# Performance work log

Measured on AMD Instinct MI355X. Metric: run time of the kernel, lower is better.

Reference implementation:

```python
import jax, jax.numpy as jnp
import numpy as np

SMU_ALPHA = 0.25
SMU_MU = 1.0e6  # repo's act.SMU default: large mu -> smooth leaky-relu (max(x, alpha*x))

def smu(x):
    a = SMU_ALPHA
    return 0.5 * ((1.0 + a) * x + (1.0 - a) * x * jax.lax.erf(SMU_MU * (1.0 - a) * x))

def setup_inputs() -> dict:
    key = jax.random.key(0)
    ks = jax.random.split(key, 6)
    B, N, D = 8, 4096, 1024
    xavier = float(np.sqrt(6.0 / (D + D)))
    def lin_w(k):
        return jax.random.uniform(k, (D, D), jnp.float32, -xavier, xavier)
    return {
        "x": jax.random.normal(ks[0], (B, N, D), jnp.float32),
        "Wvr": lin_w(ks[1]), "bvr": jnp.zeros((D,), jnp.float32),
        "Wvi": lin_w(ks[2]), "bvi": jnp.zeros((D,), jnp.float32),
        "Wk": lin_w(ks[3]), "bk": jnp.zeros((D,), jnp.float32),
        "Wq": lin_w(ks[4]), "bq": jnp.zeros((D,), jnp.float32),
    }

def reference(x, Wvr, bvr, Wvi, bvi, Wk, bk, Wq, bq):
    # real input: real and imag branches both see x
    value_real = jnp.einsum('bnd,ed->bne', x, Wvr) + bvr
    value_imag = jnp.einsum('bnd,ed->bne', x, Wvi) + bvi
    # GLU: v_real * tanh(softplus(v_imag)); dropout disabled (p=0)
    value = value_real * jnp.tanh(jax.nn.softplus(value_imag))
    key_ = jnp.einsum('bnd,ed->bne', x, Wk) + bk
    query = jnp.einsum('bnd,ed->bne', x, Wq) + bq
    # L2 normalize along the sequence dim (dim=1)
    key_n = key_ / (jnp.linalg.norm(key_, axis=1, keepdims=True) + 1e-5)
    query_n = query / (jnp.linalg.norm(query, axis=1, keepdims=True) + 1e-5)
    feature_attn = smu(jnp.einsum('bnd,bne->bde', key_n, query_n))  # [B, D, D]
    return jnp.einsum('bnd,bde->bne', value, feature_attn)
```

## Files before the change

kernel.cpp:

```cpp
#include <hip/hip_runtime.h>
#include <math.h>

typedef __bf16 bf16x8 __attribute__((ext_vector_type(8)));
typedef float f32x4 __attribute__((ext_vector_type(4)));

#define MTOT 32768
#define DD   1024
#define NSEQ 4096
#define BB   8

__device__ __forceinline__ void async16(const void* gp, void* lp) {
  __builtin_amdgcn_global_load_lds(
      (__attribute__((address_space(1))) void*)(const_cast<void*>(gp)),
      (__attribute__((address_space(3))) void*)(lp), 16, 0, 0);
}

__device__ __forceinline__ unsigned short f2bf(float f) {
  union { float f; unsigned int u; } v; v.f = f;
  unsigned int r = v.u + 0x7fffu + ((v.u >> 16) & 1u);
  return (unsigned short)(r >> 16);
}
__device__ __forceinline__ float bf2f(unsigned short u) {
  union { unsigned int u; float f; } v; v.u = ((unsigned int)u) << 16; return v.f;
}

__global__ void cvt_bf16(const float* __restrict__ in, unsigned short* __restrict__ out, int n) {
  int i = (blockIdx.x * blockDim.x + threadIdx.x) * 8;
  if (i >= n) return;
  float4 a = *(const float4*)(in + i);
  float4 b = *(const float4*)(in + i + 4);
  ushort4 o0, o1;
  o0.x = f2bf(a.x); o0.y = f2bf(a.y); o0.z = f2bf(a.z); o0.w = f2bf(a.w);
  o1.x = f2bf(b.x); o1.y = f2bf(b.y); o1.z = f2bf(b.z); o1.w = f2bf(b.w);
  *(ushort4*)(out + i) = o0;
  *(ushort4*)(out + i + 4) = o1;
}

__global__ void cvt_w(const float* __restrict__ w0, const float* __restrict__ w1,
                      const float* __restrict__ w2, const float* __restrict__ w3,
                      unsigned short* __restrict__ out) {
  int z = blockIdx.y;
  const float* in = (z == 0) ? w0 : (z == 1) ? w1 : (z == 2) ? w2 : w3;
  int i = (blockIdx.x * blockDim.x + threadIdx.x) * 8;
  float4 a = *(const float4*)(in + i);
  float4 b = *(const float4*)(in + i + 4);
  ushort4 o0, o1;
  o0.x = f2bf(a.x); o0.y = f2bf(a.y); o0.z = f2bf(a.z); o0.w = f2bf(a.w);
  o1.x = f2bf(b.x); o1.y = f2bf(b.y); o1.z = f2bf(b.z); o1.w = f2bf(b.w);
  unsigned short* o = out + (size_t)z * DD * DD;
  *(ushort4*)(o + i) = o0;
  *(ushort4*)(o + i + 4) = o1;
}

__device__ __forceinline__ void stage_half(const unsigned short* __restrict__ g,
                                           int row0, int k0,
                                           unsigned short* lds, int tid) {
#pragma unroll
  for (int l = 0; l < 2; ++l) {
    int u = l * 512 + tid;
    int r = u >> 3;
    int sl = (u & 7) ^ (r & 7);
    async16(g + (size_t)(row0 + r) * 1024 + k0 + sl * 8, (char*)lds + u * 16);
  }
}

__global__ __launch_bounds__(512, 2) void proj_all(
    const unsigned short* __restrict__ xb,
    const unsigned short* __restrict__ Wb,
    const float* __restrict__ bvr, const float* __restrict__ bvi,
    const float* __restrict__ bk,  const float* __restrict__ bq,
    unsigned short* __restrict__ oVr, unsigned short* __restrict__ oVi,
    unsigned short* __restrict__ Kt,  unsigned short* __restrict__ Qt,
    float* __restrict__ rnacc) {
  __shared__ __align__(16) unsigned short smem[65536];

  const int bx = blockIdx.x;
  const int swz = (bx & 7) * 64 + (bx >> 3);
  const int m0 = (swz >> 2) * 256;
  const int n0 = (swz & 3) * 256;
  const int z = blockIdx.z;
  const unsigned short* W = Wb + (size_t)z * DD * DD;
  const float* bias = (z == 0) ? bvr : (z == 1) ? bvi : (z == 2) ? bk : bq;

  const int tid = threadIdx.x;
  const int w = tid >> 6, lane = tid & 63;
  const int wr = w >> 2, wc = w & 3;
  const int lq = lane >> 4, lr = lane & 15;
  const int sx = lr & 7;
  const int arow0 = wr * 128 + lr;
  const int brow0 = wc * 64 + lr;

  f32x4 acc[8][4];
#pragma unroll
  for (int i = 0; i < 8; i++)
#pragma unroll
    for (int j = 0; j < 4; j++) acc[i][j] = (f32x4)(0.f);

  const int NT = 16;

  stage_half(xb, m0,       0,  smem,                     tid);
  stage_half(xb, m0 + 128, 0,  smem + 8192,              tid);
  stage_half(W,  n0,       0,  smem + 16384,             tid);
  stage_half(W,  n0 + 128, 0,  smem + 16384 + 8192,      tid);
  stage_half(W,  n0,       64, smem + 32768 + 16384,     tid);
  stage_half(W,  n0 + 128, 64, smem + 32768 + 16384 + 8192, tid);
  asm volatile("s_waitcnt vmcnt(4)" ::: "memory");
  __builtin_amdgcn_s_barrier();

  for (int t = 0; t < NT; ++t) {
    const unsigned short* As = smem + (t & 1) * 32768;
    const unsigned short* Bs = As + 16384;
    bf16x8 bfr[4][2];
#pragma unroll
    for (int q = 0; q < 4; ++q) {
      bf16x8 afq[2][2];
      if (q == 0) {
#pragma unroll
        for (int nj = 0; nj < 4; ++nj)
#pragma unroll
          for (int ks = 0; ks < 2; ++ks)
            bfr[nj][ks] = *(const bf16x8*)(Bs + (brow0 + nj * 16) * 64 +
                                           ((((ks << 2) | lq) ^ sx) << 3));
      }
#pragma unroll
      for (int mi = 0; mi < 2; ++mi)
#pragma unroll
        for (int ks = 0; ks < 2; ++ks)
          afq[mi][ks] = *(const bf16x8*)(As + (arow0 + (2 * q + mi) * 16) * 64 +
                                         ((((ks << 2) | lq) ^ sx) << 3));
      if (q == 0) {
        if (t + 1 < NT)
          stage_half(xb, m0, (t + 1) * 64, smem + ((t + 1) & 1) * 32768, tid);
      } else if (q == 1) {
        if (t + 1 < NT)
          stage_half(xb, m0 + 128, (t + 1) * 64, smem + ((t + 1) & 1) * 32768 + 8192, tid);
      } else if (q == 2) {
        if (t + 2 < NT)
          stage_half(W, n0, (t + 2) * 64, smem + (t & 1) * 32768 + 16384, tid);
      } else {
        if (t + 2 < NT)
          stage_half(W, n0 + 128, (t + 2) * 64, smem + (t & 1) * 32768 + 16384 + 8192, tid);
      }
      __builtin_amdgcn_s_barrier();
      asm volatile("s_waitcnt lgkmcnt(0)" ::: "memory");
      __builtin_amdgcn_sched_barrier(0);
      __builtin_amdgcn_s_setprio(1);
#pragma unroll
      for (int mi = 0; mi < 2; ++mi)
#pragma unroll
        for (int nj = 0; nj < 4; ++nj)
#pragma unroll
          for (int ks = 0; ks < 2; ++ks)
            acc[2 * q + mi][nj] = __builtin_amdgcn_mfma_f32_16x16x32_bf16(
                afq[mi][ks], bfr[nj][ks], acc[2 * q + mi][nj], 0, 0, 0);
      __builtin_amdgcn_s_setprio(0);
      __builtin_amdgcn_sched_barrier(0);
      if (q == 3) {
        if (t < NT - 2)       asm volatile("s_waitcnt vmcnt(4)" ::: "memory");
        else if (t == NT - 2) asm volatile("s_waitcnt vmcnt(0)" ::: "memory");
      }
      __builtin_amdgcn_s_barrier();
    }
  }

  if (z < 2) {
    unsigned short* out = (z == 0) ? oVr : oVi;
#pragma unroll
    for (int nj = 0; nj < 4; ++nj) {
      int col = n0 + wc * 64 + nj * 16 + lr;
      float bv = bias[col];
#pragma unroll
      for (int mrep = 0; mrep < 8; ++mrep) {
        int rowb = m0 + wr * 128 + mrep * 16 + lq * 4;
#pragma unroll
        for (int r = 0; r < 4; ++r)
          out[(size_t)(rowb + r) * DD + col] = f2bf(acc[mrep][nj][r] + bv);
      }
    }
  } else {
    unsigned short* outp = (z == 2) ? Kt : Qt;
    const int which = z - 2;
    const int b = m0 >> 12;
    const int nbase = m0 & 4095;
    float* racc = rnacc + which * (BB * DD) + b * DD;
    unsigned short* T = smem;
    const int SP2 = 264;
#pragma unroll
    for (int ch = 0; ch < 2; ++ch) {
      if ((wc >> 1) == ch) {
#pragma unroll
        for (int nj = 0; nj < 4; ++nj) {
          int cloc = (wc & 1) * 64 + nj * 16 + lr;
          float bv = bias[n0 + ch * 128 + cloc];
#pragma unroll
          for (int mrep = 0; mrep < 8; ++mrep) {
            int rowb = wr * 128 + mrep * 16 + lq * 4;
            ushort4 pk;
            pk.x = f2bf(acc[mrep][nj][0] + bv); pk.y = f2bf(acc[mrep][nj][1] + bv);
            pk.z = f2bf(acc[mrep][nj][2] + bv); pk.w = f2bf(acc[mrep][nj][3] + bv);
            *(ushort4*)(T + cloc * SP2 + rowb) = pk;
          }
        }
      }
      __syncthreads();
#pragma unroll
      for (int p = 0; p < 8; ++p) {
        int dl = p * 16 + (tid >> 5);
        int nc = (tid & 31) * 8;
        ushort4 v0 = *(const ushort4*)(T + dl * SP2 + nc);
        ushort4 v1 = *(const ushort4*)(T + dl * SP2 + nc + 4);
        int d = n0 + ch * 128 + dl;
        *(ushort4*)(outp + (size_t)(b * DD + d) * NSEQ + nbase + nc)     = v0;
        *(ushort4*)(outp + (size_t)(b * DD + d) * NSEQ + nbase + nc + 4) = v1;
        float s = bf2f(v0.x)*bf2f(v0.x) + bf2f(v0.y)*bf2f(v0.y) + bf2f(v0.z)*bf2f(v0.z) + bf2f(v0.w)*bf2f(v0.w)
                + bf2f(v1.x)*bf2f(v1.x) + bf2f(v1.y)*bf2f(v1.y) + bf2f(v1.z)*bf2f(v1.z) + bf2f(v1.w)*bf2f(v1.w);
#pragma unroll
        for (int off = 1; off < 32; off <<= 1) s += __shfl_xor(s, off, 32);
        if ((tid & 31) == 0) atomicAdd(&racc[d], s);
      }
      __syncthreads();
    }
  }
}

__global__ void finalize_rn(float* __restrict__ rn) {
  int i = blockIdx.x * blockDim.x + threadIdx.x;
  rn[i] = 1.f / (sqrtf(rn[i]) + 1e-5f);
}

__global__ void glu(unsigned short* __restrict__ V, const unsigned short* __restrict__ Vi, int n) {
  int i = (blockIdx.x * blockDim.x + threadIdx.x) * 8;
  if (i >= n) return;
  ushort4 r0 = *(const ushort4*)(V + i);
  ushort4 r1 = *(const ushort4*)(V + i + 4);
  ushort4 i0 = *(const ushort4*)(Vi + i);
  ushort4 i1 = *(const ushort4*)(Vi + i + 4);
  unsigned short vr[8] = {r0.x, r0.y, r0.z, r0.w, r1.x, r1.y, r1.z, r1.w};
  unsigned short vi[8] = {i0.x, i0.y, i0.z, i0.w, i1.x, i1.y, i1.z, i1.w};
  unsigned short o[8];
#pragma unroll
  for (int k = 0; k < 8; k++) {
    float a = bf2f(vr[k]), b = bf2f(vi[k]);
    float g;
    if (b > 10.f) g = 1.f;
    else { float t = __expf(b); float u = t * (t + 2.f); g = u / (u + 2.f); }
    o[k] = f2bf(a * g);
  }
  *(ushort4*)(V + i)     = make_ushort4(o[0], o[1], o[2], o[3]);
  *(ushort4*)(V + i + 4) = make_ushort4(o[4], o[5], o[6], o[7]);
}

__global__ __launch_bounds__(256) void attn_gemm(
    const unsigned short* __restrict__ Qt, const unsigned short* __restrict__ Kt,
    const float* __restrict__ rn, unsigned short* __restrict__ fat) {
  const int b = blockIdx.z;
  const int e0 = blockIdx.y * 128;
  const int d0 = blockIdx.x * 128;
  const unsigned short* A  = Qt + (size_t)b * DD * NSEQ;
  const unsigned short* Bm = Kt + (size_t)b * DD * NSEQ;
  unsigned short* out = fat + (size_t)b * DD * DD;

  __shared__ __align__(16) unsigned short As[128 * 32];
  __shared__ __align__(16) unsigned short Bs[128 * 32];

  const int tid = threadIdx.x;
  const int w = tid >> 6, lane = tid & 63;
  const int wm = w >> 1, wn = w & 1;
  const int lq = lane >> 4, lr = lane & 15;
  const int srow = lane >> 2, scol = (lane & 3) * 8;

  f32x4 acc[4][4];
#pragma unroll
  for (int i = 0; i < 4; i++)
#pragma unroll
    for (int j = 0; j < 4; j++) acc[i][j] = (f32x4)(0.f);

  for (int k0 = 0; k0 < NSEQ; k0 += 32) {
#pragma unroll
    for (int s = 0; s < 2; s++) {
      int c = w * 2 + s;
      int row = c * 16 + srow;
      async16(A  + (size_t)(e0 + row) * NSEQ + k0 + scol, (char*)As + c * 1024 + lane * 16);
      async16(Bm + (size_t)(d0 + row) * NSEQ + k0 + scol, (char*)Bs + c * 1024 + lane * 16);
    }
    __syncthreads();
    bf16x8 af[4], bfr[4];
#pragma unroll
    for (int i = 0; i < 4; i++) af[i]  = *(const bf16x8*)(As + (wm * 64 + i * 16 + lr) * 32 + lq * 8);
#pragma unroll
    for (int j = 0; j < 4; j++) bfr[j] = *(const bf16x8*)(Bs + (wn * 64 + j * 16 + lr) * 32 + lq * 8);
#pragma unroll
    for (int i = 0; i < 4; i++)
#pragma unroll
      for (int j = 0; j < 4; j++)
        acc[i][j] = __builtin_amdgcn_mfma_f32_16x16x32_bf16(af[i], bfr[j], acc[i][j], 0, 0, 0);
    __syncthreads();
  }
#pragma unroll
  for (int j = 0; j < 4; j++) {
    int col = d0 + wn * 64 + j * 16 + lr;
    float rk = rn[b * DD + col];
#pragma unroll
    for (int i = 0; i < 4; i++) {
      int rowb = e0 + wm * 64 + i * 16 + lq * 4;
#pragma unroll
      for (int r = 0; r < 4; r++) {
        float rq = rn[BB * DD + b * DD + rowb + r];
        float c = acc[i][j][r] * rq * rk;
        c = (c > 0.f) ? c : 0.25f * c;
        out[(size_t)(rowb + r) * DD + col] = f2bf(c);
      }
    }
  }
}

__global__ __launch_bounds__(512, 2) void out_gemm(
    const unsigned short* __restrict__ V, const unsigned short* __restrict__ fat,
    float* __restrict__ out) {
  __shared__ __align__(16) unsigned short smem[65536];

  const int bx = blockIdx.x;
  const int swz = (bx & 7) * 64 + (bx >> 3);
  const int m0 = (swz >> 2) * 256;
  const int e0 = (swz & 3) * 256;
  const int b = m0 >> 12;
  const unsigned short* Bm = fat + (size_t)b * DD * DD;

  const int tid = threadIdx.x;
  const int w = tid >> 6, lane = tid & 63;
  const int wr = w >> 2, wc = w & 3;
  const int lq = lane >> 4, lr = lane & 15;
  const int sx = lr & 7;
  const int arow0 = wr * 128 + lr;
  const int brow0 = wc * 64 + lr;

  f32x4 acc[8][4];
#pragma unroll
  for (int i = 0; i < 8; i++)
#pragma unroll
    for (int j = 0; j < 4; j++) acc[i][j] = (f32x4)(0.f);

  const int NT = 16;

  stage_half(V,  m0,       0,  smem,                        tid);
  stage_half(V,  m0 + 128, 0,  smem + 8192,                 tid);
  stage_half(Bm, e0,       0,  smem + 16384,                tid);
  stage_half(Bm, e0 + 128, 0,  smem + 16384 + 8192,         tid);
  stage_half(Bm, e0,       64, smem + 32768 + 16384,        tid);
  stage_half(Bm, e0 + 128, 64, smem + 32768 + 16384 + 8192, tid);
  asm volatile("s_waitcnt vmcnt(4)" ::: "memory");
  __builtin_amdgcn_s_barrier();

  for (int t = 0; t < NT; ++t) {
    const unsigned short* As = smem + (t & 1) * 32768;
    const unsigned short* Bs = As + 16384;
    bf16x8 bfr[4][2];
#pragma unroll
    for (int q = 0; q < 4; ++q) {
      bf16x8 afq[2][2];
      if (q == 0) {
#pragma unroll
        for (int nj = 0; nj < 4; ++nj)
#pragma unroll
          for (int ks = 0; ks < 2; ++ks)
            bfr[nj][ks] = *(const bf16x8*)(Bs + (brow0 + nj * 16) * 64 +
                                           ((((ks << 2) | lq) ^ sx) << 3));
      }
#pragma unroll
      for (int mi = 0; mi < 2; ++mi)
#pragma unroll
        for (int ks = 0; ks < 2; ++ks)
          afq[mi][ks] = *(const bf16x8*)(As + (arow0 + (2 * q + mi) * 16) * 64 +
                                         ((((ks << 2) | lq) ^ sx) << 3));
      if (q == 0) {
        if (t + 1 < NT)
          stage_half(V, m0, (t + 1) * 64, smem + ((t + 1) & 1) * 32768, tid);
      } else if (q == 1) {
        if (t + 1 < NT)
          stage_half(V, m0 + 128, (t + 1) * 64, smem + ((t + 1) & 1) * 32768 + 8192, tid);
      } else if (q == 2) {
        if (t + 2 < NT)
          stage_half(Bm, e0, (t + 2) * 64, smem + (t & 1) * 32768 + 16384, tid);
      } else {
        if (t + 2 < NT)
          stage_half(Bm, e0 + 128, (t + 2) * 64, smem + (t & 1) * 32768 + 16384 + 8192, tid);
      }
      __builtin_amdgcn_s_barrier();
      asm volatile("s_waitcnt lgkmcnt(0)" ::: "memory");
      __builtin_amdgcn_sched_barrier(0);
      __builtin_amdgcn_s_setprio(1);
#pragma unroll
      for (int mi = 0; mi < 2; ++mi)
#pragma unroll
        for (int nj = 0; nj < 4; ++nj)
#pragma unroll
          for (int ks = 0; ks < 2; ++ks)
            acc[2 * q + mi][nj] = __builtin_amdgcn_mfma_f32_16x16x32_bf16(
                afq[mi][ks], bfr[nj][ks], acc[2 * q + mi][nj], 0, 0, 0);
      __builtin_amdgcn_s_setprio(0);
      __builtin_amdgcn_sched_barrier(0);
      if (q == 3) {
        if (t < NT - 2)       asm volatile("s_waitcnt vmcnt(4)" ::: "memory");
        else if (t == NT - 2) asm volatile("s_waitcnt vmcnt(0)" ::: "memory");
      }
      __builtin_amdgcn_s_barrier();
    }
  }

#pragma unroll
  for (int nj = 0; nj < 4; ++nj) {
    int col = e0 + wc * 64 + nj * 16 + lr;
#pragma unroll
    for (int mrep = 0; mrep < 8; ++mrep) {
      int rowb = m0 + wr * 128 + mrep * 16 + lq * 4;
#pragma unroll
      for (int r = 0; r < 4; ++r)
        out[(size_t)(rowb + r) * DD + col] = acc[mrep][nj][r];
    }
  }
}

extern "C" void kernel_launch(void* const* d_in, const int* in_sizes, int n_in,
                              void* d_out, int out_size, void* d_ws, size_t ws_size,
                              hipStream_t stream) {
  const float* x   = (const float*)d_in[0];
  const float* Wvr = (const float*)d_in[1];
  const float* bvr = (const float*)d_in[2];
  const float* Wvi = (const float*)d_in[3];
  const float* bvi = (const float*)d_in[4];
  const float* Wk  = (const float*)d_in[5];
  const float* bk  = (const float*)d_in[6];
  const float* Wq  = (const float*)d_in[7];
  const float* bq  = (const float*)d_in[8];
  float* out = (float*)d_out;

  char* p = (char*)d_ws;
  unsigned short* xb  = (unsigned short*)p; p += (size_t)MTOT * DD * 2;
  unsigned short* Wb  = (unsigned short*)p; p += 4ull * DD * DD * 2;
  unsigned short* Kt  = (unsigned short*)p; p += (size_t)BB * DD * NSEQ * 2;
  unsigned short* Qt  = (unsigned short*)p; p += (size_t)BB * DD * NSEQ * 2;
  unsigned short* Vb  = (unsigned short*)p; p += (size_t)MTOT * DD * 2;
  unsigned short* fat = (unsigned short*)p; p += (size_t)BB * DD * DD * 2;
  float* rn = (float*)p; p += 2ull * BB * DD * sizeof(float);

  unsigned short* ViBuf = (unsigned short*)d_out;

  int nx = MTOT * DD;
  int nw = DD * DD;
  cvt_bf16<<<nx / 8 / 256, 256, 0, stream>>>(x, xb, nx);
  cvt_w<<<dim3(nw / 8 / 256, 4), 256, 0, stream>>>(Wvr, Wvi, Wk, Wq, Wb);
  hipMemsetAsync(rn, 0, 2ull * BB * DD * sizeof(float), stream);

  proj_all<<<dim3(512, 1, 4), 512, 0, stream>>>(
      xb, Wb, bvr, bvi, bk, bq, Vb, ViBuf, Kt, Qt, rn);

  glu<<<nx / 8 / 256, 256, 0, stream>>>(Vb, ViBuf, nx);
  finalize_rn<<<2 * BB * DD / 256, 256, 0, stream>>>(rn);

  attn_gemm<<<dim3(DD / 128, DD / 128, BB), 256, 0, stream>>>(Qt, Kt, rn, fat);
  out_gemm<<<dim3(512), 512, 0, stream>>>(Vb, fat, out);
}
```

Measured before the change: 775.6 us.

## Pipeline attn_gemm with swizzled double-buffered LDS and inline-asm LDS reads

Rewrites the feature-attention GEMM from a simple 128x128 tile with sync-per-k-step into a 256x128 tile, 512-thread kernel that uses XOR-swizzled double-buffered LDS, staged async global-to-LDS loads overlapped with MFMA, and prefetch two k-steps ahead. It also replaces pointer-based LDS fragment reads in all GEMMs with precomputed byte offsets and explicit ds_read_b128 asm, toggling the buffer by XOR. The goal is to hide global latency and cut address arithmetic; it raises LDS use and register pressure and depends on hand-placed waitcnts being correct.

```diff
diff --git a/kernel.cpp b/kernel.cpp
--- a/kernel.cpp
+++ b/kernel.cpp
@@ -22,6 +22,16 @@
 }
 __device__ __forceinline__ float bf2f(unsigned short u) {
   union { unsigned int u; float f; } v; v.u = ((unsigned int)u) << 16; return v.f;
+}
+
+__device__ __forceinline__ unsigned lds_off(void* p) {
+  return (unsigned)(unsigned long long)
+      (__attribute__((address_space(3))) void*)p;
+}
+__device__ __forceinline__ bf16x8 dsr128(unsigned a) {
+  bf16x8 r;
+  asm volatile("ds_read_b128 %0, %1" : "=v"(r) : "v"(a));
+  return r;
 }
 
 __global__ void cvt_bf16(const float* __restrict__ in, unsigned short* __restrict__ out, int n) {
@@ -52,6 +62,7 @@
   *(ushort4*)(o + i + 4) = o1;
 }
 
+template<int LDG>
 __device__ __forceinline__ void stage_half(const unsigned short* __restrict__ g,
                                            int row0, int k0,
                                            unsigned short* lds, int tid) {
@@ -60,7 +71,7 @@
     int u = l * 512 + tid;
     int r = u >> 3;
     int sl = (u & 7) ^ (r & 7);
-    async16(g + (size_t)(row0 + r) * 1024 + k0 + sl * 8, (char*)lds + u * 16);
+    async16(g + (size_t)(row0 + r) * LDG + k0 + sl * 8, (char*)lds + u * 16);
   }
 }
 
@@ -98,48 +109,52 @@
 
   const int NT = 16;
 
-  stage_half(xb, m0,       0,  smem,                     tid);
-  stage_half(xb, m0 + 128, 0,  smem + 8192,              tid);
-  stage_half(W,  n0,       0,  smem + 16384,             tid);
-  stage_half(W,  n0 + 128, 0,  smem + 16384 + 8192,      tid);
-  stage_half(W,  n0,       64, smem + 32768 + 16384,     tid);
-  stage_half(W,  n0 + 128, 64, smem + 32768 + 16384 + 8192, tid);
+  const unsigned sbase = lds_off(smem);
+  const unsigned sw0 = (unsigned)((lq ^ sx) << 4);
+  const unsigned sw1 = (unsigned)(((4 | lq) ^ sx) << 4);
+  unsigned aA0 = sbase + arow0 * 128 + sw0;
+  unsigned aA1 = sbase + arow0 * 128 + sw1;
+  unsigned aB0 = sbase + 32768 + brow0 * 128 + sw0;
+  unsigned aB1 = sbase + 32768 + brow0 * 128 + sw1;
+
+  stage_half<1024>(xb, m0,       0,  smem,                     tid);
+  stage_half<1024>(xb, m0 + 128, 0,  smem + 8192,              tid);
+  stage_half<1024>(W,  n0,       0,  smem + 16384,             tid);
+  stage_half<1024>(W,  n0 + 128, 0,  smem + 16384 + 8192,      tid);
+  stage_half<1024>(W,  n0,       64, smem + 32768 + 16384,     tid);
+  stage_half<1024>(W,  n0 + 128, 64, smem + 32768 + 16384 + 8192, tid);
   asm volatile("s_waitcnt vmcnt(4)" ::: "memory");
   __builtin_amdgcn_s_barrier();
 
   for (int t = 0; t < NT; ++t) {
-    const unsigned short* As = smem + (t & 1) * 32768;
-    const unsigned short* Bs = As + 16384;
     bf16x8 bfr[4][2];
 #pragma unroll
     for (int q = 0; q < 4; ++q) {
       bf16x8 afq[2][2];
       if (q == 0) {
 #pragma unroll
-        for (int nj = 0; nj < 4; ++nj)
-#pragma unroll
-          for (int ks = 0; ks < 2; ++ks)
-            bfr[nj][ks] = *(const bf16x8*)(Bs + (brow0 + nj * 16) * 64 +
-                                           ((((ks << 2) | lq) ^ sx) << 3));
-      }
-#pragma unroll
-      for (int mi = 0; mi < 2; ++mi)
-#pragma unroll
-        for (int ks = 0; ks < 2; ++ks)
-          afq[mi][ks] = *(const bf16x8*)(As + (arow0 + (2 * q + mi) * 16) * 64 +
-                                         ((((ks << 2) | lq) ^ sx) << 3));
+        for (int nj = 0; nj < 4; ++nj) {
+          bfr[nj][0] = dsr128(aB0 + nj * 2048u);
+          bfr[nj][1] = dsr128(aB1 + nj * 2048u);
+        }
+      }
+#pragma unroll
+      for (int mi = 0; mi < 2; ++mi) {
+        afq[mi][0] = dsr128(aA0 + (2 * q + mi) * 2048u);
+        afq[mi][1] = dsr128(aA1 + (2 * q + mi) * 2048u);
+      }
       if (q == 0) {
         if (t + 1 < NT)
-          stage_half(xb, m0, (t + 1) * 64, smem + ((t + 1) & 1) * 32768, tid);
+          stage_half<1024>(xb, m0, (t + 1) * 64, smem + ((t + 1) & 1) * 32768, tid);
       } else if (q == 1) {
         if (t + 1 < NT)
-          stage_half(xb, m0 + 128, (t + 1) * 64, smem + ((t + 1) & 1) * 32768 + 8192, tid);
+          stage_half<1024>(xb, m0 + 128, (t + 1) * 64, smem + ((t + 1) & 1) * 32768 + 8192, tid);
       } else if (q == 2) {
         if (t + 2 < NT)
-          stage_half(W, n0, (t + 2) * 64, smem + (t & 1) * 32768 + 16384, tid);
+          stage_half<1024>(W, n0, (t + 2) * 64, smem + (t & 1) * 32768 + 16384, tid);
       } else {
         if (t + 2 < NT)
-          stage_half(W, n0 + 128, (t + 2) * 64, smem + (t & 1) * 32768 + 16384 + 8192, tid);
+          stage_half<1024>(W, n0 + 128, (t + 2) * 64, smem + (t & 1) * 32768 + 16384 + 8192, tid);
       }
       __builtin_amdgcn_s_barrier();
       asm volatile("s_waitcnt lgkmcnt(0)" ::: "memory");
@@ -161,6 +176,7 @@
       }
       __builtin_amdgcn_s_barrier();
     }
+    aA0 ^= 65536u; aA1 ^= 65536u; aB0 ^= 65536u; aB1 ^= 65536u;
   }
 
   if (z < 2) {
@@ -250,24 +266,25 @@
   *(ushort4*)(V + i + 4) = make_ushort4(o[4], o[5], o[6], o[7]);
 }
 
-__global__ __launch_bounds__(256) void attn_gemm(
+__global__ __launch_bounds__(512, 2) void attn_gemm(
     const unsigned short* __restrict__ Qt, const unsigned short* __restrict__ Kt,
     const float* __restrict__ rn, unsigned short* __restrict__ fat) {
+  __shared__ __align__(16) unsigned short smem[57344];
+
   const int b = blockIdx.z;
-  const int e0 = blockIdx.y * 128;
   const int d0 = blockIdx.x * 128;
+  const int e0 = blockIdx.y * 256;
   const unsigned short* A  = Qt + (size_t)b * DD * NSEQ;
   const unsigned short* Bm = Kt + (size_t)b * DD * NSEQ;
   unsigned short* out = fat + (size_t)b * DD * DD;
 
-  __shared__ __align__(16) unsigned short As[128 * 32];
-  __shared__ __align__(16) unsigned short Bs[128 * 32];
-
   const int tid = threadIdx.x;
   const int w = tid >> 6, lane = tid & 63;
-  const int wm = w >> 1, wn = w & 1;
+  const int wr = w >> 1, wc = w & 1;
   const int lq = lane >> 4, lr = lane & 15;
-  const int srow = lane >> 2, scol = (lane & 3) * 8;
+  const int sx = lr & 7;
+  const int arow0 = wr * 64 + lr;
+  const int brow0 = wc * 64 + lr;
 
   f32x4 acc[4][4];
 #pragma unroll
@@ -275,38 +292,79 @@
 #pragma unroll
     for (int j = 0; j < 4; j++) acc[i][j] = (f32x4)(0.f);
 
-  for (int k0 = 0; k0 < NSEQ; k0 += 32) {
-#pragma unroll
-    for (int s = 0; s < 2; s++) {
-      int c = w * 2 + s;
-      int row = c * 16 + srow;
-      async16(A  + (size_t)(e0 + row) * NSEQ + k0 + scol, (char*)As + c * 1024 + lane * 16);
-      async16(Bm + (size_t)(d0 + row) * NSEQ + k0 + scol, (char*)Bs + c * 1024 + lane * 16);
-    }
-    __syncthreads();
-    bf16x8 af[4], bfr[4];
-#pragma unroll
-    for (int i = 0; i < 4; i++) af[i]  = *(const bf16x8*)(As + (wm * 64 + i * 16 + lr) * 32 + lq * 8);
-#pragma unroll
-    for (int j = 0; j < 4; j++) bfr[j] = *(const bf16x8*)(Bs + (wn * 64 + j * 16 + lr) * 32 + lq * 8);
-#pragma unroll
-    for (int i = 0; i < 4; i++)
-#pragma unroll
-      for (int j = 0; j < 4; j++)
-        acc[i][j] = __builtin_amdgcn_mfma_f32_16x16x32_bf16(af[i], bfr[j], acc[i][j], 0, 0, 0);
-    __syncthreads();
-  }
-#pragma unroll
-  for (int j = 0; j < 4; j++) {
-    int col = d0 + wn * 64 + j * 16 + lr;
+  const int NT = 64;
+
+  const unsigned sbase = lds_off(smem);
+  const unsigned sw0 = (unsigned)((lq ^ sx) << 4);
+  const unsigned sw1 = (unsigned)(((4 | lq) ^ sx) << 4);
+  unsigned aA0 = sbase + arow0 * 128 + sw0;
+  unsigned aA1 = sbase + arow0 * 128 + sw1;
+  unsigned aB0 = sbase + 32768 + brow0 * 128 + sw0;
+  unsigned aB1 = sbase + 32768 + brow0 * 128 + sw1;
+
+  stage_half<NSEQ>(A,  e0,       0,  smem,                 tid);
+  stage_half<NSEQ>(A,  e0 + 128, 0,  smem + 8192,          tid);
+  stage_half<NSEQ>(Bm, d0,       0,  smem + 16384,         tid);
+  stage_half<NSEQ>(Bm, d0,       64, smem + 32768 + 16384, tid);
+  asm volatile("s_waitcnt vmcnt(2)" ::: "memory");
+  __builtin_amdgcn_s_barrier();
+
+  for (int t = 0; t < NT; ++t) {
+    bf16x8 bfr[4][2];
+#pragma unroll
+    for (int q = 0; q < 4; ++q) {
+      bf16x8 afq[2];
+      if (q == 0) {
+#pragma unroll
+        for (int nj = 0; nj < 4; ++nj) {
+          bfr[nj][0] = dsr128(aB0 + nj * 2048u);
+          bfr[nj][1] = dsr128(aB1 + nj * 2048u);
+        }
+      }
+      afq[0] = dsr128(aA0 + q * 2048u);
+      afq[1] = dsr128(aA1 + q * 2048u);
+      if (q == 0) {
+        if (t + 1 < NT)
+          stage_half<NSEQ>(A, e0, (t + 1) * 64, smem + ((t + 1) & 1) * 32768, tid);
+      } else if (q == 1) {
+        if (t + 1 < NT)
+          stage_half<NSEQ>(A, e0 + 128, (t + 1) * 64, smem + ((t + 1) & 1) * 32768 + 8192, tid);
+      } else if (q == 2) {
+        if (t + 2 < NT)
+          stage_half<NSEQ>(Bm, d0, (t + 2) * 64, smem + (t & 1) * 32768 + 16384, tid);
+      }
+      __builtin_amdgcn_s_barrier();
+      asm volatile("s_waitcnt lgkmcnt(0)" ::: "memory");
+      __builtin_amdgcn_sched_barrier(0);
+      __builtin_amdgcn_s_setprio(1);
+#pragma unroll
+      for (int nj = 0; nj < 4; ++nj)
+#pragma unroll
+        for (int ks = 0; ks < 2; ++ks)
+          acc[q][nj] = __builtin_amdgcn_mfma_f32_16x16x32_bf16(
+              afq[ks], bfr[nj][ks], acc[q][nj], 0, 0, 0);
+      __builtin_amdgcn_s_setprio(0);
+      __builtin_amdgcn_sched_barrier(0);
+      if (q == 3) {
+        if (t < NT - 2)       asm volatile("s_waitcnt vmcnt(2)" ::: "memory");
+        else if (t == NT - 2) asm volatile("s_waitcnt vmcnt(0)" ::: "memory");
+      }
+      __builtin_amdgcn_s_barrier();
+    }
+    aA0 ^= 65536u; aA1 ^= 65536u; aB0 ^= 65536u; aB1 ^= 65536u;
+  }
+
+#pragma unroll
+  for (int nj = 0; nj < 4; ++nj) {
+    int col = d0 + wc * 64 + nj * 16 + lr;
     float rk = rn[b * DD + col];
 #pragma unroll
-    for (int i = 0; i < 4; i++) {
-      int rowb = e0 + wm * 64 + i * 16 + lq * 4;
-#pragma unroll
-      for (int r = 0; r < 4; r++) {
+    for (int mi = 0; mi < 4; ++mi) {
+      int rowb = e0 + wr * 64 + mi * 16 + lq * 4;
+#pragma unroll
+      for (int r = 0; r < 4; ++r) {
         float rq = rn[BB * DD + b * DD + rowb + r];
-        float c = acc[i][j][r] * rq * rk;
+        float c = acc[mi][nj][r] * rq * rk;
         c = (c > 0.f) ? c : 0.25f * c;
         out[(size_t)(rowb + r) * DD + col] = f2bf(c);
       }
@@ -342,48 +400,52 @@
 
   const int NT = 16;
 
-  stage_half(V,  m0,       0,  smem,                        tid);
-  stage_half(V,  m0 + 128, 0,  smem + 8192,                 tid);
-  stage_half(Bm, e0,       0,  smem + 16384,                tid);
-  stage_half(Bm, e0 + 128, 0,  smem + 16384 + 8192,         tid);
-  stage_half(Bm, e0,       64, smem + 32768 + 16384,        tid);
-  stage_half(Bm, e0 + 128, 64, smem + 32768 + 16384 + 8192, tid);
+  const unsigned sbase = lds_off(smem);
+  const unsigned sw0 = (unsigned)((lq ^ sx) << 4);
+  const unsigned sw1 = (unsigned)(((4 | lq) ^ sx) << 4);
+  unsigned aA0 = sbase + arow0 * 128 + sw0;
+  unsigned aA1 = sbase + arow0 * 128 + sw1;
+  unsigned aB0 = sbase + 32768 + brow0 * 128 + sw0;
+  unsigned aB1 = sbase + 32768 + brow0 * 128 + sw1;
+
+  stage_half<1024>(V,  m0,       0,  smem,                        tid);
+  stage_half<1024>(V,  m0 + 128, 0,  smem + 8192,                 tid);
+  stage_half<1024>(Bm, e0,       0,  smem + 16384,                tid);
+  stage_half<1024>(Bm, e0 + 128, 0,  smem + 16384 + 8192,         tid);
+  stage_half<1024>(Bm, e0,       64, smem + 32768 + 16384,        tid);
+  stage_half<1024>(Bm, e0 + 128, 64, smem + 32768 + 16384 + 8192, tid);
   asm volatile("s_waitcnt vmcnt(4)" ::: "memory");
   __builtin_amdgcn_s_barrier();
 
   for (int t = 0; t < NT; ++t) {
-    const unsigned short* As = smem + (t & 1) * 32768;
-    const unsigned short* Bs = As + 16384;
     bf16x8 bfr[4][2];
 #pragma unroll
     for (int q = 0; q < 4; ++q) {
       bf16x8 afq[2][2];
       if (q == 0) {
 #pragma unroll
-        for (int nj = 0; nj < 4; ++nj)
-#pragma unroll
-          for (int ks = 0; ks < 2; ++ks)
-            bfr[nj][ks] = *(const bf16x8*)(Bs + (brow0 + nj * 16) * 64 +
-                                           ((((ks << 2) | lq) ^ sx) << 3));
-      }
-#pragma unroll
-      for (int mi = 0; mi < 2; ++mi)
-#pragma unroll
-        for (int ks = 0; ks < 2; ++ks)
-          afq[mi][ks] = *(const bf16x8*)(As + (arow0 + (2 * q + mi) * 16) * 64 +
-                                         ((((ks << 2) | lq) ^ sx) << 3));
+        for (int nj = 0; nj < 4; ++nj) {
+          bfr[nj][0] = dsr128(aB0 + nj * 2048u);
+          bfr[nj][1] = dsr128(aB1 + nj * 2048u);
+        }
+      }
+#pragma unroll
+      for (int mi = 0; mi < 2; ++mi) {
+        afq[mi][0] = dsr128(aA0 + (2 * q + mi) * 2048u);
+        afq[mi][1] = dsr128(aA1 + (2 * q + mi) * 2048u);
+      }
       if (q == 0) {
         if (t + 1 < NT)
-          stage_half(V, m0, (t + 1) * 64, smem + ((t + 1) & 1) * 32768, tid);
+          stage_half<1024>(V, m0, (t + 1) * 64, smem + ((t + 1) & 1) * 32768, tid);
       } else if (q == 1) {
         if (t + 1 < NT)
-          stage_half(V, m0 + 128, (t + 1) * 64, smem + ((t + 1) & 1) * 32768 + 8192, tid);
+          stage_half<1024>(V, m0 + 128, (t + 1) * 64, smem + ((t + 1) & 1) * 32768 + 8192, tid);
       } else if (q == 2) {
         if (t + 2 < NT)
-          stage_half(Bm, e0, (t + 2) * 64, smem + (t & 1) * 32768 + 16384, tid);
+          stage_half<1024>(Bm, e0, (t + 2) * 64, smem + (t & 1) * 32768 + 16384, tid);
       } else {
         if (t + 2 < NT)
-          stage_half(Bm, e0 + 128, (t + 2) * 64, smem + (t & 1) * 32768 + 16384 + 8192, tid);
+          stage_half<1024>(Bm, e0 + 128, (t + 2) * 64, smem + (t & 1) * 32768 + 16384 + 8192, tid);
       }
       __builtin_amdgcn_s_barrier();
       asm volatile("s_waitcnt lgkmcnt(0)" ::: "memory");
@@ -405,6 +467,7 @@
       }
       __builtin_amdgcn_s_barrier();
     }
+    aA0 ^= 65536u; aA1 ^= 65536u; aB0 ^= 65536u; aB1 ^= 65536u;
   }
 
 #pragma unroll
@@ -457,6 +520,6 @@
   glu<<<nx / 8 / 256, 256, 0, stream>>>(Vb, ViBuf, nx);
   finalize_rn<<<2 * BB * DD / 256, 256, 0, stream>>>(rn);
 
-  attn_gemm<<<dim3(DD / 128, DD / 128, BB), 256, 0, stream>>>(Qt, Kt, rn, fat);
+  attn_gemm<<<dim3(DD / 128, DD / 256, BB), 512, 0, stream>>>(Qt, Kt, rn, fat);
   out_gemm<<<dim3(512), 512, 0, stream>>>(Vb, fat, out);
 }
```

After: 738.8 us. 4.7% less time.
